# Optimization experiments

Measured on AMD Instinct MI355X. Metric: run time of the kernel, lower is better.

The kernel has to match this reference:

```python
import jax, jax.numpy as jnp
import numpy as np

K = 16
BN_EPS = 1e-5


def _knn_cosine(x, k):
    # x: [B,P,D] -> neighbor indices [B,P,k], largest cosine similarity, no self-loops
    xn = x * jax.lax.rsqrt(jnp.sum(x * x, -1, keepdims=True) + 1e-12)
    sim = jnp.einsum('bpd,bqd->bpq', xn, xn)
    P = x.shape[1]
    sim = sim - 1e9 * jnp.eye(P, dtype=sim.dtype)
    return jax.lax.top_k(sim, k)[1]


def _edge_conv(x, k, wa, ba, g, b, m, v, wb, bb):
    # to_undirected(knn_graph(cosine)) + EdgeConv(nn([x_i, x_j - x_i]), aggr='add')
    B, P, D = x.shape
    nbr = _knn_cosine(x, k)                            # [B,P,k] j in knn(i)
    nbr2 = jax.vmap(lambda n: n[n])(nbr)               # [B,P,k,k] knn of each neighbor
    mutual = jnp.any(nbr2 == jnp.arange(P)[None, :, None, None], -1)  # [B,P,k]
    xj = jax.vmap(lambda xb, nb: xb[nb])(x, nbr)       # [B,P,k,D]
    xi = jnp.broadcast_to(x[:, :, None, :], xj.shape)

    def msg(e):
        h = e @ wa + ba
        h = (h - m) * jax.lax.rsqrt(v + BN_EPS) * g + b  # BatchNorm1d (eval)
        h = jax.nn.relu(h)
        return jax.nn.relu(h @ wb + bb)

    # directed knn edges j->i: message aggregated at center i
    mA = msg(jnp.concatenate([xi, xj - xi], -1)).sum(2)  # [B,P,H]
    # reverse edges i->j added by to_undirected; drop duplicates (mutual pairs)
    mB = msg(jnp.concatenate([xj, xi - xj], -1)) * (~mutual)[..., None].astype(x.dtype)
    H = mB.shape[-1]
    scat = jax.vmap(
        lambda idx, mm: jnp.zeros((P, H), mm.dtype).at[idx.reshape(-1)].add(mm.reshape(-1, H))
    )(nbr, mB)
    return mA + scat


def reference(x, datanorm, iw1, ib1, iw2, ib2, iw3, ib3,
              c1wa, c1ba, c1g, c1b, c1m, c1v, c1wb, c1bb,
              c2wa, c2ba, c2g, c2b, c2m, c2v, c2wb, c2bb,
              c3wa, c3ba, c3g, c3b, c3m, c3v, c3wb, c3bb,
              ow1, ob1, ow2, ob2, ow3, ob3):
    h = datanorm * x
    h = jax.nn.relu(h @ iw1 + ib1)
    h = jax.nn.relu(h @ iw2 + ib2)
    h = jax.nn.relu(h @ iw3 + ib3)               # [B,P,64]
    orig = h
    h = _edge_conv(h, K, c1wa, c1ba, c1g, c1b, c1m, c1v, c1wb, c1bb)
    h = jnp.concatenate([h, orig], -1)           # [B,P,128]
    res1 = h
    h = _edge_conv(h, K, c2wa, c2ba, c2g, c2b, c2m, c2v, c2wb, c2bb)
    h = jnp.concatenate([h, res1], -1)           # [B,P,192]
    res2 = h
    h = _edge_conv(h, K, c3wa, c3ba, c3g, c3b, c3m, c3v, c3wb, c3bb)
    h = jnp.concatenate([h, res2], -1)           # [B,P,256]
    pooled = h.max(axis=1)                       # global_max_pool -> [B,256]
    o = jax.nn.relu(pooled @ ow1 + ob1)
    o = jax.nn.relu(o @ ow2 + ob2)
    o = o @ ow3 + ob3
    return (o.squeeze(-1), h)


def setup_inputs() -> dict:
    key = jax.random.key(0)
    ks = iter(jax.random.split(key, 64))
    B, P, F, H = 16, 1024, 5, 64

    def W(shape, s=0.1):
        return jax.random.normal(next(ks), shape, jnp.float32) * s

    inp = {
        'x': jax.random.normal(next(ks), (B, P, F), jnp.float32),
        'datanorm': jnp.ones((F,), jnp.float32),
        'iw1': W((F, 2 * H)), 'ib1': jnp.zeros((2 * H,), jnp.float32),
        'iw2': W((2 * H, 2 * H)), 'ib2': jnp.zeros((2 * H,), jnp.float32),
        'iw3': W((2 * H, H)), 'ib3': jnp.zeros((H,), jnp.float32),
    }
    mid = 3 * H // 2
    for i, din in zip((1, 2, 3), (2 * H, 4 * H, 6 * H)):
        inp[f'c{i}wa'] = W((din, mid))
        inp[f'c{i}ba'] = jnp.zeros((mid,), jnp.float32)
        inp[f'c{i}g'] = jnp.ones((mid,), jnp.float32)
        inp[f'c{i}b'] = jnp.zeros((mid,), jnp.float32)
        inp[f'c{i}m'] = jnp.zeros((mid,), jnp.float32)
        inp[f'c{i}v'] = jnp.ones((mid,), jnp.float32)
        inp[f'c{i}wb'] = W((mid, H))
        inp[f'c{i}bb'] = jnp.zeros((H,), jnp.float32)
    inp['ow1'] = W((4 * H, 2 * H)); inp['ob1'] = jnp.zeros((2 * H,), jnp.float32)
    inp['ow2'] = W((2 * H, H // 2)); inp['ob2'] = jnp.zeros((H // 2,), jnp.float32)
    inp['ow3'] = W((H // 2, 1)); inp['ob3'] = jnp.zeros((1,), jnp.float32)
    return inp
```

## Files before the change

### kernel.cpp

```cpp
#include <hip/hip_runtime.h>
#include <hip/hip_bf16.h>

#define B 16
#define P 1024
#define NPT 16384
#define KNN 16
#define MID 96
#define HD 64

#define WS_UV   0
#define WS_RN   (WS_UV + NPT*192)
#define WS_NBR  (WS_RN + NPT)
#define WS_WUV  (WS_NBR + NPT*KNN)
#define WS_CVEC (WS_WUV + 192*192)
#define WS_PART (WS_CVEC + 96)
#define WS_XT   (WS_PART + 16*16*256)

#define NCH 2

typedef float f32x2 __attribute__((ext_vector_type(2)));

__device__ __forceinline__ void pk_lo(f32x2 &acc, f32x2 c, f32x2 r) {
    asm("v_pk_fma_f32 %0, %1, %2, %0 op_sel:[0,0,0] op_sel_hi:[1,0,1]"
        : "+v"(acc) : "v"(c), "v"(r));
}
__device__ __forceinline__ void pk_hi(f32x2 &acc, f32x2 c, f32x2 r) {
    asm("v_pk_fma_f32 %0, %1, %2, %0 op_sel:[0,1,0] op_sel_hi:[1,1,1]"
        : "+v"(acc) : "v"(c), "v"(r));
}

__global__ void k_input(const float* __restrict__ x, const float* __restrict__ dn,
                        const float* __restrict__ w1, const float* __restrict__ b1,
                        const float* __restrict__ w2, const float* __restrict__ b2,
                        const float* __restrict__ w3, const float* __restrict__ b3,
                        float* __restrict__ Hout) {
    __shared__ float xs[8][5];
    __shared__ float t1[8][128];
    __shared__ float t2[8][128];
    int tid = threadIdx.x;
    int p0 = blockIdx.x * 8;
    if (tid < 40) { int p = tid / 5, f = tid - p * 5; xs[p][f] = x[(p0 + p) * 5 + f] * dn[f]; }
    __syncthreads();
    int c = tid;
    {
        float bb = b1[c];
        #pragma unroll
        for (int p = 0; p < 8; p++) {
            float a = bb;
            #pragma unroll
            for (int f = 0; f < 5; f++) a += xs[p][f] * w1[f * 128 + c];
            t1[p][c] = fmaxf(a, 0.f);
        }
    }
    __syncthreads();
    {
        float acc[8];
        float bb = b2[c];
        #pragma unroll
        for (int p = 0; p < 8; p++) acc[p] = bb;
        for (int k = 0; k < 128; k++) {
            float w = w2[k * 128 + c];
            #pragma unroll
            for (int p = 0; p < 8; p++) acc[p] += t1[p][k] * w;
        }
        #pragma unroll
        for (int p = 0; p < 8; p++) t2[p][c] = fmaxf(acc[p], 0.f);
    }
    __syncthreads();
    if (c < 64) {
        float acc[8];
        float bb = b3[c];
        #pragma unroll
        for (int p = 0; p < 8; p++) acc[p] = bb;
        for (int k = 0; k < 128; k++) {
            float w = w3[k * 64 + c];
            #pragma unroll
            for (int p = 0; p < 8; p++) acc[p] += t2[p][k] * w;
        }
        #pragma unroll
        for (int p = 0; p < 8; p++) Hout[(p0 + p) * 256 + 192 + c] = fmaxf(acc[p], 0.f);
    }
}

__global__ void k_prep(const float* __restrict__ wa, const float* __restrict__ ba,
                       const float* __restrict__ g, const float* __restrict__ bB,
                       const float* __restrict__ m, const float* __restrict__ v,
                       int D, float* __restrict__ WUV, float* __restrict__ cvec) {
    int idx = blockIdx.x * 256 + threadIdx.x;
    if (idx < D * 192) {
        int k = idx / 192, col = idx - k * 192;
        int ch = (col < 96) ? col : col - 96;
        float s = g[ch] * rsqrtf(v[ch] + 1e-5f);
        float w = (col < 96) ? (wa[k * 96 + ch] - wa[(D + k) * 96 + ch]) : wa[(D + k) * 96 + ch];
        WUV[idx] = w * s;
    }
    if (blockIdx.x == 0 && threadIdx.x < 96) {
        int ch = threadIdx.x;
        float s = g[ch] * rsqrtf(v[ch] + 1e-5f);
        cvec[ch] = ba[ch] * s + (bB[ch] - m[ch] * s);
    }
}

__global__ void __launch_bounds__(256) k_tr(const float* __restrict__ Hout, int colOff, int D,
                                            float* __restrict__ Xt) {
    __shared__ float t[64][65];
    int tid = threadIdx.x;
    int d0 = blockIdx.x * 64, p0 = blockIdx.y * 64, b = blockIdx.z;
    int r4 = tid >> 6, c = tid & 63;
    #pragma unroll
    for (int k = 0; k < 16; k++) {
        int row = k * 4 + r4;
        t[row][c] = Hout[(size_t)(b * P + p0 + row) * 256 + colOff + d0 + c];
    }
    __syncthreads();
    #pragma unroll
    for (int k = 0; k < 16; k++) {
        int d = k * 4 + r4;
        Xt[((size_t)b * D + d0 + d) * 1024 + p0 + c] = t[c][d];
    }
}

__global__ void k_rn2(const float* __restrict__ Xt, int D, float* __restrict__ rn) {
    int p = blockIdx.x * 256 + threadIdx.x;
    if (p >= NPT) return;
    int b = p >> 10, pp = p & 1023;
    const float* base = Xt + (size_t)b * D * 1024 + pp;
    float ss = 0.f;
    for (int d = 0; d < D; d++) { float v = base[(size_t)d * 1024]; ss += v * v; }
    rn[p] = rsqrtf(ss + 1e-12f);
}

#define ST_LD 520

__device__ __forceinline__ unsigned long long packkey(float v, int q) {
    unsigned u = __float_as_uint(v);
    u = (u & 0x80000000u) ? ~u : (u | 0x80000000u);
    return ((unsigned long long)u << 32) | (unsigned)(1023 - q);
}

template<int D>
__global__ void __launch_bounds__(256) k_knn3(const float* __restrict__ Xt,
                                              const float* __restrict__ rn,
                                              unsigned long long* __restrict__ pkeys) {
    __shared__ __align__(16) float sbuf[16 * ST_LD];
    float* XiT = sbuf;
    float* simtile = sbuf;
    int tid = threadIdx.x;
    int chunk = blockIdx.x & 1, rt = (blockIdx.x >> 1) & 63, b = blockIdx.x >> 7;
    int i0 = rt * 16, q0 = chunk * 512;
    int lane = tid & 63, w = tid >> 6;
    for (int idx = tid; idx < 16 * D; idx += 256) {
        int d = idx >> 4, r = idx & 15;
        XiT[d * 16 + r] = Xt[((size_t)b * D + d) * 1024 + i0 + r];
    }
    __syncthreads();
    const float* cvb = Xt + (size_t)b * D * 1024 + q0 + 8 * lane;
    f32x2 accA[4] = {}, accB[4] = {}, accC[4] = {}, accD[4] = {};
    #pragma unroll 4
    for (int d = 0; d < D; d++) {
        float4 cv0 = *(const float4*)(cvb + (size_t)d * 1024);
        float4 cv1 = *(const float4*)(cvb + (size_t)d * 1024 + 4);
        float4 rv = *(const float4*)(XiT + d * 16 + 4 * w);
        f32x2 cA = {cv0.x, cv0.y}, cB = {cv0.z, cv0.w};
        f32x2 cC = {cv1.x, cv1.y}, cD = {cv1.z, cv1.w};
        f32x2 rAB = {rv.x, rv.y}, rCD = {rv.z, rv.w};
        pk_lo(accA[0], cA, rAB); pk_lo(accB[0], cB, rAB); pk_lo(accC[0], cC, rAB); pk_lo(accD[0], cD, rAB);
        pk_hi(accA[1], cA, rAB); pk_hi(accB[1], cB, rAB); pk_hi(accC[1], cC, rAB); pk_hi(accD[1], cD, rAB);
        pk_lo(accA[2], cA, rCD); pk_lo(accB[2], cB, rCD); pk_lo(accC[2], cC, rCD); pk_lo(accD[2], cD, rCD);
        pk_hi(accA[3], cA, rCD); pk_hi(accB[3], cB, rCD); pk_hi(accC[3], cC, rCD); pk_hi(accD[3], cD, rCD);
    }
    __syncthreads();
    float4 rq0 = *(const float4*)(rn + b * P + q0 + 8 * lane);
    float4 rq1 = *(const float4*)(rn + b * P + q0 + 8 * lane + 4);
    int qg = q0 + 8 * lane;
    #pragma unroll
    for (int r = 0; r < 4; r++) {
        float rnir = rn[b * P + i0 + 4 * w + r];
        int ig = i0 + 4 * w + r;
        float4 v0, v1;
        v0.x = accA[r].x * rnir * rq0.x;
        v0.y = accA[r].y * rnir * rq0.y;
        v0.z = accB[r].x * rnir * rq0.z;
        v0.w = accB[r].y * rnir * rq0.w;
        v1.x = accC[r].x * rnir * rq1.x;
        v1.y = accC[r].y * rnir * rq1.y;
        v1.z = accD[r].x * rnir * rq1.z;
        v1.w = accD[r].y * rnir * rq1.w;
        if (qg + 0 == ig) v0.x = -1e9f;
        if (qg + 1 == ig) v0.y = -1e9f;
        if (qg + 2 == ig) v0.z = -1e9f;
        if (qg + 3 == ig) v0.w = -1e9f;
        if (qg + 4 == ig) v1.x = -1e9f;
        if (qg + 5 == ig) v1.y = -1e9f;
        if (qg + 6 == ig) v1.z = -1e9f;
        if (qg + 7 == ig) v1.w = -1e9f;
        *(float4*)(simtile + (4 * w + r) * ST_LD + 8 * lane) = v0;
        *(float4*)(simtile + (4 * w + r) * ST_LD + 8 * lane + 4) = v1;
    }
    __syncthreads();
    int g = lane >> 4, lane16 = lane & 15;
    int row = w * 4 + g;
    int sh = lane & 48;
    unsigned long long listkey = 0ull;
    for (int t = 0; t < 8; t++) {
        int qb = q0 + t * 64;
        unsigned long long c0 = packkey(simtile[row * ST_LD + t * 64 + lane16     ], qb + lane16);
        unsigned long long c1 = packkey(simtile[row * ST_LD + t * 64 + lane16 + 16], qb + lane16 + 16);
        unsigned long long c2 = packkey(simtile[row * ST_LD + t * 64 + lane16 + 32], qb + lane16 + 32);
        unsigned long long c3 = packkey(simtile[row * ST_LD + t * 64 + lane16 + 48], qb + lane16 + 48);
        unsigned long long lmin = __shfl(listkey, 15, 16);
        unsigned long long b0 = __ballot(c0 > lmin);
        unsigned long long b1 = __ballot(c1 > lmin);
        unsigned long long b2 = __ballot(c2 > lmin);
        unsigned long long b3 = __ballot(c3 > lmin);
        unsigned long long gm = ((b0 >> sh) & 0xFFFFull)
                              | (((b1 >> sh) & 0xFFFFull) << 16)
                              | (((b2 >> sh) & 0xFFFFull) << 32)
                              | (((b3 >> sh) & 0xFFFFull) << 48);
        while (gm) {
            int pb = __builtin_ctzll(gm);
            gm &= gm - 1;
            int slot = pb >> 4, src = pb & 15;
            unsigned long long sel = (slot & 2) ? ((slot & 1) ? c3 : c2)
                                                : ((slot & 1) ? c1 : c0);
            unsigned long long mv = __shfl(sel, src, 16);
            unsigned long long bal = __ballot(listkey > mv);
            int pos = __popcll((bal >> sh) & 0xFFFFull);
            unsigned long long up = __shfl_up(listkey, 1, 16);
            if (lane16 == pos) listkey = mv;
            else if (lane16 > pos) listkey = up;
        }
    }
    pkeys[(((size_t)(b * P + i0 + row)) * NCH + chunk) * 16 + lane16] = listkey;
}

__global__ void __launch_bounds__(256) k_knn_merge(const unsigned long long* __restrict__ pkeys,
                                                   int* __restrict__ nbr) {
    int tid = threadIdx.x;
    int lane = tid & 63, w = tid >> 6;
    int g = lane >> 4, lane16 = lane & 15;
    int row = blockIdx.x * 16 + w * 4 + g;
    int sh = lane & 48;
    unsigned long long listkey = pkeys[((size_t)row * NCH + 0) * 16 + lane16];
    #pragma unroll
    for (int s = 1; s < NCH; s++) {
        unsigned long long cand = pkeys[((size_t)row * NCH + s) * 16 + lane16];
        unsigned long long lmin = __shfl(listkey, 15, 16);
        unsigned long long bal = __ballot(cand > lmin);
        unsigned long long gm = (bal >> sh) & 0xFFFFull;
        while (gm) {
            int src = __builtin_ctzll(gm);
            gm &= gm - 1;
            unsigned long long mv = __shfl(cand, src, 16);
            unsigned long long bal2 = __ballot(listkey > mv);
            int pos = __popcll((bal2 >> sh) & 0xFFFFull);
            unsigned long long up = __shfl_up(listkey, 1, 16);
            if (lane16 == pos) listkey = mv;
            else if (lane16 > pos) listkey = up;
        }
    }
    nbr[(size_t)row * KNN + lane16] = 1023 - (int)(listkey & 0xFFFFFFFFull);
}

__global__ void k_uv(const float* __restrict__ Hout, int colOff, int D,
                     const float* __restrict__ WUV, float* __restrict__ UV) {
    __shared__ __align__(16) float Xt[16 * 192];
    int tid = threadIdx.x;
    int p0 = blockIdx.x * 16;
    for (int idx = tid; idx < 16 * D; idx += 192) {
        int r = idx / D, d = idx - r * D;
        Xt[r * 192 + d] = Hout[(p0 + r) * 256 + colOff + d];
    }
    __syncthreads();
    float acc[16];
    #pragma unroll
    for (int p = 0; p < 16; p++) acc[p] = 0.f;
    for (int k = 0; k < D; k += 4) {
        float w0 = WUV[(k + 0) * 192 + tid];
        float w1 = WUV[(k + 1) * 192 + tid];
        float w2 = WUV[(k + 2) * 192 + tid];
        float w3 = WUV[(k + 3) * 192 + tid];
        #pragma unroll
        for (int p = 0; p < 16; p++) {
            float4 xv = *(const float4*)(Xt + p * 192 + k);
            acc[p] += xv.x * w0;
            acc[p] += xv.y * w1;
            acc[p] += xv.z * w2;
            acc[p] += xv.w * w3;
        }
    }
    #pragma unroll
    for (int p = 0; p < 16; p++) UV[(size_t)(p0 + p) * 192 + tid] = acc[p];
}

__global__ void __launch_bounds__(256) k_edge(const float* __restrict__ UV, const int* __restrict__ nbr,
                                              const float* __restrict__ wb, const float* __restrict__ bbv,
                                              const float* __restrict__ cvec, int colOut,
                                              float* __restrict__ Hout) {
    __shared__ __align__(16) f32x2 msg2[4][96];
    __shared__ float cvs[96];
    __shared__ float bbs[64];
    int tid = threadIdx.x;
    int w = tid >> 6, lane = tid & 63;
    float wreg[96];
    #pragma unroll
    for (int k = 0; k < 96; k++) wreg[k] = wb[k * 64 + lane];
    if (tid < 96) cvs[tid] = cvec[tid];
    if (tid < 64) bbs[tid] = bbv[tid];
    int ifl = blockIdx.x * 4 + w;
    int b = ifl >> 10, i = ifl & 1023;
    const float* Ui = UV + (size_t)ifl * 192;
    float ui0 = Ui[lane];
    float ui1 = (lane < 32) ? Ui[64 + lane] : 0.f;
    float vi0 = Ui[96 + lane];
    float vi1 = (lane < 32) ? Ui[160 + lane] : 0.f;
    int jv = nbr[ifl * KNN + (lane & 15)];
    int jk = __shfl(jv, lane >> 2, 64);
    const int4* nb4p = (const int4*)(nbr + ((size_t)b * P + jk) * KNN + (lane & 3) * 4);
    int4 nb4 = *nb4p;
    bool hit = (nb4.x == i) | (nb4.y == i) | (nb4.z == i) | (nb4.w == i);
    unsigned long long mb = __ballot(hit);
    mb |= (mb >> 1); mb |= (mb >> 2);
    float accA = 0.f;
    __syncthreads();
    float bbl = bbs[lane];
    float cv0 = cvs[lane];
    float cv1 = (lane < 32) ? cvs[64 + lane] : 0.f;
    f32x2* mrow = msg2[w];
    const float4* mq = (const float4*)mrow;
    f32x2 ai0 = {ui0, vi0};
    f32x2 ai1 = {ui1, vi1};
    f32x2 cc0 = {cv0, cv0};
    f32x2 cc1 = {cv1, cv1};
    int jf = b * P + __shfl(jv, 0, 64);
    const float* Uj = UV + (size_t)jf * 192;
    float pu0 = Uj[lane];
    float pu1 = (lane < 32) ? Uj[64 + lane] : 0.f;
    float pv0 = Uj[96 + lane];
    float pv1 = (lane < 32) ? Uj[160 + lane] : 0.f;
    for (int kk = 0; kk < KNN; kk++) {
        float cu0 = pu0, cu1 = pu1, cw0 = pv0, cw1 = pv1;
        int jfc = jf;
        if (kk + 1 < KNN) {
            jf = b * P + __shfl(jv, kk + 1, 64);
            const float* Un = UV + (size_t)jf * 192;
            pu0 = Un[lane];
            pu1 = (lane < 32) ? Un[64 + lane] : 0.f;
            pv0 = Un[96 + lane];
            pv1 = (lane < 32) ? Un[160 + lane] : 0.f;
        }
        {
            f32x2 s0 = {cw0, cu0};
            f32x2 m0 = ai0 + s0 + cc0;
            m0.x = fmaxf(m0.x, 0.f);
            m0.y = fmaxf(m0.y, 0.f);
            mrow[lane] = m0;
            if (lane < 32) {
                f32x2 s1 = {cw1, cu1};
                f32x2 m1 = ai1 + s1 + cc1;
                m1.x = fmaxf(m1.x, 0.f);
                m1.y = fmaxf(m1.y, 0.f);
                mrow[64 + lane] = m1;
            }
        }
        f32x2 t0 = {bbl, bbl};
        f32x2 t1 = {0.f, 0.f};
        f32x2 t2 = {0.f, 0.f};
        f32x2 t3 = {0.f, 0.f};
        #pragma unroll
        for (int k8 = 0; k8 < 12; k8++) {
            float4 qa = mq[4 * k8 + 0];
            float4 qb = mq[4 * k8 + 1];
            float4 qc = mq[4 * k8 + 2];
            float4 qd = mq[4 * k8 + 3];
            t0 += (f32x2){qa.x, qa.y} * (f32x2){wreg[8 * k8 + 0], wreg[8 * k8 + 0]};
            t0 += (f32x2){qa.z, qa.w} * (f32x2){wreg[8 * k8 + 1], wreg[8 * k8 + 1]};
            t1 += (f32x2){qb.x, qb.y} * (f32x2){wreg[8 * k8 + 2], wreg[8 * k8 + 2]};
            t1 += (f32x2){qb.z, qb.w} * (f32x2){wreg[8 * k8 + 3], wreg[8 * k8 + 3]};
            t2 += (f32x2){qc.x, qc.y} * (f32x2){wreg[8 * k8 + 4], wreg[8 * k8 + 4]};
            t2 += (f32x2){qc.z, qc.w} * (f32x2){wreg[8 * k8 + 5], wreg[8 * k8 + 5]};
            t3 += (f32x2){qd.x, qd.y} * (f32x2){wreg[8 * k8 + 6], wreg[8 * k8 + 6]};
            t3 += (f32x2){qd.z, qd.w} * (f32x2){wreg[8 * k8 + 7], wreg[8 * k8 + 7]};
        }
        f32x2 tt = (t0 + t1) + (t2 + t3);
        accA += fmaxf(tt.x, 0.f);
        if (!((mb >> (4 * kk)) & 1))
            atomicAdd(&Hout[(size_t)jfc * 256 + colOut + lane], fmaxf(tt.y, 0.f));
    }
    atomicAdd(&Hout[(size_t)ifl * 256 + colOut + lane], accA);
}

__global__ void k_pool(const float* __restrict__ Hout, float* __restrict__ part) {
    int tid = threadIdx.x;
    int b = blockIdx.x >> 4, pt = blockIdx.x & 15;
    float mv = -1e30f;
    for (int p = pt * 64; p < pt * 64 + 64; p++)
        mv = fmaxf(mv, Hout[(size_t)(b * P + p) * 256 + tid]);
    part[(b * 16 + pt) * 256 + tid] = mv;
}

__global__ void k_out(const float* __restrict__ part,
                      const float* __restrict__ w1, const float* __restrict__ b1,
                      const float* __restrict__ w2, const float* __restrict__ b2,
                      const float* __restrict__ w3, const float* __restrict__ b3,
                      float* __restrict__ out) {
    __shared__ float pooled[256];
    __shared__ float r1[128];
    __shared__ float r2[32];
    int tid = threadIdx.x, b = blockIdx.x;
    float mv = -1e30f;
    for (int t = 0; t < 16; t++) mv = fmaxf(mv, part[(b * 16 + t) * 256 + tid]);
    pooled[tid] = mv;
    __syncthreads();
    if (tid < 128) {
        float a = b1[tid];
        for (int k = 0; k < 256; k++) a += pooled[k] * w1[k * 128 + tid];
        r1[tid] = fmaxf(a, 0.f);
    }
    __syncthreads();
    if (tid < 32) {
        float a = b2[tid];
        for (int k = 0; k < 128; k++) a += r1[k] * w2[k * 32 + tid];
        r2[tid] = fmaxf(a, 0.f);
    }
    __syncthreads();
    if (tid == 0) {
        float a = b3[0];
        for (int k = 0; k < 32; k++) a += r2[k] * w3[k];
        out[b] = a;
    }
}

extern "C" void kernel_launch(void* const* d_in, const int* in_sizes, int n_in,
                              void* d_out, int out_size, void* d_ws, size_t ws_size,
                              hipStream_t stream) {
    const float* x  = (const float*)d_in[0];
    const float* dn = (const float*)d_in[1];
    float* out = (float*)d_out;
    float* Hout = out + 16;
    float* ws = (float*)d_ws;
    float* UV   = ws + WS_UV;
    float* rn   = ws + WS_RN;
    int*   nbr  = (int*)(ws + WS_NBR);
    float* WUV  = ws + WS_WUV;
    float* cvec = ws + WS_CVEC;
    float* part = ws + WS_PART;
    float* Xt   = ws + WS_XT;
    unsigned long long* pkeys = (unsigned long long*)UV;

    hipMemsetAsync(d_out, 0, (size_t)out_size * sizeof(float), stream);

    k_input<<<2048, 128, 0, stream>>>(x, dn,
        (const float*)d_in[2], (const float*)d_in[3],
        (const float*)d_in[4], (const float*)d_in[5],
        (const float*)d_in[6], (const float*)d_in[7], Hout);

    const int convOff[3] = {192, 128, 64};
    const int convD[3]   = {64, 128, 192};
    const int convOut[3] = {128, 64, 0};
    for (int c = 0; c < 3; c++) {
        int pb = 8 + c * 8;
        const float* wa  = (const float*)d_in[pb + 0];
        const float* ba  = (const float*)d_in[pb + 1];
        const float* g   = (const float*)d_in[pb + 2];
        const float* bB  = (const float*)d_in[pb + 3];
        const float* m   = (const float*)d_in[pb + 4];
        const float* v   = (const float*)d_in[pb + 5];
        const float* wb  = (const float*)d_in[pb + 6];
        const float* bbv = (const float*)d_in[pb + 7];
        int D = convD[c], off = convOff[c], co = convOut[c];
        k_prep<<<(D * 192 + 255) / 256, 256, 0, stream>>>(wa, ba, g, bB, m, v, D, WUV, cvec);
        k_tr<<<dim3(D / 64, P / 64, B), 256, 0, stream>>>(Hout, off, D, Xt);
        k_rn2<<<64, 256, 0, stream>>>(Xt, D, rn);
        if (c == 0)      k_knn3<64><<<2048, 256, 0, stream>>>(Xt, rn, pkeys);
        else if (c == 1) k_knn3<128><<<2048, 256, 0, stream>>>(Xt, rn, pkeys);
        else             k_knn3<192><<<2048, 256, 0, stream>>>(Xt, rn, pkeys);
        k_knn_merge<<<1024, 256, 0, stream>>>(pkeys, nbr);
        k_uv<<<1024, 192, 0, stream>>>(Hout, off, D, WUV, UV);
        k_edge<<<4096, 256, 0, stream>>>(UV, nbr, wb, bbv, cvec, co, Hout);
    }

    k_pool<<<256, 256, 0, stream>>>(Hout, part);
    k_out<<<16, 256, 0, stream>>>(part,
        (const float*)d_in[32], (const float*)d_in[33],
        (const float*)d_in[34], (const float*)d_in[35],
        (const float*)d_in[36], (const float*)d_in[37], out);
}
```

Baseline: 1.109 ms.

## Double-buffer edge message rows in LDS and pipeline neighbor loads two ahead

The edge kernel now keeps two LDS message buffers per wavefront. It writes the next neighbor's hidden message into one buffer while the GEMV reads the other, with global loads issued two neighbors ahead, and the loop is fully unrolled. The aim is to overlap the LDS write, the global gather latency and the GEMV, instead of serializing them on each iteration. It also adds a launch-bounds occupancy hint of 4, which may constrain the 96-float weight registers and cause spills. LDS use per block doubles.

```diff
diff --git a/kernel.cpp b/kernel.cpp
--- a/kernel.cpp
+++ b/kernel.cpp
@@ -293,11 +293,12 @@
     for (int p = 0; p < 16; p++) UV[(size_t)(p0 + p) * 192 + tid] = acc[p];
 }
 
-__global__ void __launch_bounds__(256) k_edge(const float* __restrict__ UV, const int* __restrict__ nbr,
-                                              const float* __restrict__ wb, const float* __restrict__ bbv,
-                                              const float* __restrict__ cvec, int colOut,
-                                              float* __restrict__ Hout) {
-    __shared__ __align__(16) f32x2 msg2[4][96];
+__global__ void __launch_bounds__(256, 4) k_edge(const float* __restrict__ UV, const int* __restrict__ nbr,
+                                                 const float* __restrict__ wb, const float* __restrict__ bbv,
+                                                 const float* __restrict__ cvec, int colOut,
+                                                 float* __restrict__ Hout) {
+    __shared__ __align__(16) f32x2 msgA[4][96];
+    __shared__ __align__(16) f32x2 msgB[4][96];
     __shared__ float cvs[96];
     __shared__ float bbs[64];
     int tid = threadIdx.x;
@@ -326,43 +327,26 @@
     float bbl = bbs[lane];
     float cv0 = cvs[lane];
     float cv1 = (lane < 32) ? cvs[64 + lane] : 0.f;
-    f32x2* mrow = msg2[w];
-    const float4* mq = (const float4*)mrow;
     f32x2 ai0 = {ui0, vi0};
     f32x2 ai1 = {ui1, vi1};
     f32x2 cc0 = {cv0, cv0};
     f32x2 cc1 = {cv1, cv1};
-    int jf = b * P + __shfl(jv, 0, 64);
-    const float* Uj = UV + (size_t)jf * 192;
-    float pu0 = Uj[lane];
-    float pu1 = (lane < 32) ? Uj[64 + lane] : 0.f;
-    float pv0 = Uj[96 + lane];
-    float pv1 = (lane < 32) ? Uj[160 + lane] : 0.f;
-    for (int kk = 0; kk < KNN; kk++) {
-        float cu0 = pu0, cu1 = pu1, cw0 = pv0, cw1 = pv1;
-        int jfc = jf;
-        if (kk + 1 < KNN) {
-            jf = b * P + __shfl(jv, kk + 1, 64);
-            const float* Un = UV + (size_t)jf * 192;
-            pu0 = Un[lane];
-            pu1 = (lane < 32) ? Un[64 + lane] : 0.f;
-            pv0 = Un[96 + lane];
-            pv1 = (lane < 32) ? Un[160 + lane] : 0.f;
-        }
-        {
-            f32x2 s0 = {cw0, cu0};
-            f32x2 m0 = ai0 + s0 + cc0;
-            m0.x = fmaxf(m0.x, 0.f);
-            m0.y = fmaxf(m0.y, 0.f);
-            mrow[lane] = m0;
-            if (lane < 32) {
-                f32x2 s1 = {cw1, cu1};
-                f32x2 m1 = ai1 + s1 + cc1;
-                m1.x = fmaxf(m1.x, 0.f);
-                m1.y = fmaxf(m1.y, 0.f);
-                mrow[64 + lane] = m1;
-            }
-        }
+    auto MSG = [&](f32x2* mrow, float cu0, float cu1, float cw0, float cw1) {
+        f32x2 s0 = {cw0, cu0};
+        f32x2 m0 = ai0 + s0 + cc0;
+        m0.x = fmaxf(m0.x, 0.f);
+        m0.y = fmaxf(m0.y, 0.f);
+        mrow[lane] = m0;
+        if (lane < 32) {
+            f32x2 s1 = {cw1, cu1};
+            f32x2 m1 = ai1 + s1 + cc1;
+            m1.x = fmaxf(m1.x, 0.f);
+            m1.y = fmaxf(m1.y, 0.f);
+            mrow[64 + lane] = m1;
+        }
+    };
+    auto GEMV = [&](const f32x2* mrowc) -> f32x2 {
+        const float4* mq = (const float4*)mrowc;
         f32x2 t0 = {bbl, bbl};
         f32x2 t1 = {0.f, 0.f};
         f32x2 t2 = {0.f, 0.f};
@@ -382,10 +366,58 @@
             t3 += (f32x2){qd.x, qd.y} * (f32x2){wreg[8 * k8 + 6], wreg[8 * k8 + 6]};
             t3 += (f32x2){qd.z, qd.w} * (f32x2){wreg[8 * k8 + 7], wreg[8 * k8 + 7]};
         }
-        f32x2 tt = (t0 + t1) + (t2 + t3);
-        accA += fmaxf(tt.x, 0.f);
+        return (t0 + t1) + (t2 + t3);
+    };
+    int jf0 = b * P + __shfl(jv, 0, 64);
+    {
+        const float* U0 = UV + (size_t)jf0 * 192;
+        float au0 = U0[lane];
+        float au1 = (lane < 32) ? U0[64 + lane] : 0.f;
+        float av0 = U0[96 + lane];
+        float av1 = (lane < 32) ? U0[160 + lane] : 0.f;
+        MSG(msgA[w], au0, au1, av0, av1);
+    }
+    int jf1 = b * P + __shfl(jv, 1, 64);
+    float bu0, bu1, bv0, bv1;
+    {
+        const float* U1 = UV + (size_t)jf1 * 192;
+        bu0 = U1[lane];
+        bu1 = (lane < 32) ? U1[64 + lane] : 0.f;
+        bv0 = U1[96 + lane];
+        bv1 = (lane < 32) ? U1[160 + lane] : 0.f;
+    }
+    float au0, au1, av0, av1;
+    #pragma unroll
+    for (int kk = 0; kk < KNN; kk += 2) {
+        int jfcA = jf0;
+        if (kk + 2 < KNN) {
+            jf0 = b * P + __shfl(jv, kk + 2, 64);
+            const float* Un = UV + (size_t)jf0 * 192;
+            au0 = Un[lane];
+            au1 = (lane < 32) ? Un[64 + lane] : 0.f;
+            av0 = Un[96 + lane];
+            av1 = (lane < 32) ? Un[160 + lane] : 0.f;
+        }
+        MSG(msgB[w], bu0, bu1, bv0, bv1);
+        f32x2 ttA = GEMV(msgA[w]);
+        accA += fmaxf(ttA.x, 0.f);
         if (!((mb >> (4 * kk)) & 1))
-            atomicAdd(&Hout[(size_t)jfc * 256 + colOut + lane], fmaxf(tt.y, 0.f));
+            atomicAdd(&Hout[(size_t)jfcA * 256 + colOut + lane], fmaxf(ttA.y, 0.f));
+        int jfcB = jf1;
+        if (kk + 3 < KNN) {
+            jf1 = b * P + __shfl(jv, kk + 3, 64);
+            const float* Un = UV + (size_t)jf1 * 192;
+            bu0 = Un[lane];
+            bu1 = (lane < 32) ? Un[64 + lane] : 0.f;
+            bv0 = Un[96 + lane];
+            bv1 = (lane < 32) ? Un[160 + lane] : 0.f;
+        }
+        if (kk + 2 < KNN)
+            MSG(msgA[w], au0, au1, av0, av1);
+        f32x2 ttB = GEMV(msgB[w]);
+        accA += fmaxf(ttB.x, 0.f);
+        if (!((mb >> (4 * (kk + 1))) & 1))
+            atomicAdd(&Hout[(size_t)jfcB * 256 + colOut + lane], fmaxf(ttB.y, 0.f));
     }
     atomicAdd(&Hout[(size_t)ifl * 256 + colOut + lane], accA);
 }
```

Result: slower. 4.280 ms (+285.7%).
